# Optimization experiments

Measured on AMD Instinct MI355X. Metric: run time of the kernel, lower is better.

Reference implementation:

```python
import jax, jax.numpy as jnp
import numpy as np

N_NODES = 100000
HIDDEN = 128


def gcn_conv(x, edge_index, W, b, n_nodes):
    """PyG GCNConv: out = D^{-1/2} (A+I) D^{-1/2} (x @ W) + b."""
    src, dst = edge_index[0], edge_index[1]
    # add self-loops
    loop = jnp.arange(n_nodes, dtype=src.dtype)
    src = jnp.concatenate([src, loop])
    dst = jnp.concatenate([dst, loop])
    # degree of (A + I) w.r.t. destination nodes
    deg = jax.ops.segment_sum(jnp.ones_like(dst, dtype=x.dtype), dst,
                              num_segments=n_nodes)
    dinv = jax.lax.rsqrt(jnp.where(deg > 0, deg, 1.0))
    norm = dinv[src] * dinv[dst]  # [E+N]
    h = x @ W                      # [N, F_out]
    msg = h[src] * norm[:, None]   # gather + scale, [E+N, F_out]
    out = jax.ops.segment_sum(msg, dst, num_segments=n_nodes)
    return out + b


def setup_inputs() -> dict:
    key = jax.random.key(0)
    k1, k2, k3, k4, k5, k6 = jax.random.split(key, 6)
    num_features, num_classes = 128, 40
    n_edges = 1600000
    x = jax.random.normal(k1, (N_NODES, num_features), dtype=jnp.float32)
    edge_index = jax.random.randint(k2, (2, n_edges), 0, N_NODES, dtype=jnp.int64)
    s1 = 1.0 / np.sqrt(num_features)
    s2 = 1.0 / np.sqrt(HIDDEN)
    W1 = jax.random.uniform(k3, (num_features, HIDDEN), jnp.float32, -s1, s1)
    b1 = jax.random.uniform(k4, (HIDDEN,), jnp.float32, -s1, s1)
    W2 = jax.random.uniform(k5, (HIDDEN, num_classes), jnp.float32, -s2, s2)
    b2 = jax.random.uniform(k6, (num_classes,), jnp.float32, -s2, s2)
    return {"x": x, "edge_index": edge_index, "W1": W1, "b1": b1,
            "W2": W2, "b2": b2}


def reference(x, edge_index, W1, b1, W2, b2):
    n = x.shape[0]
    h = gcn_conv(x, edge_index, W1, b1, n)
    h = jax.nn.relu(h)
    # dropout is identity in eval mode (training=False)
    out = gcn_conv(h, edge_index, W2, b2, n)
    return out
```

## Files before the change

kernel.cpp:

```cpp
#include <hip/hip_runtime.h>


__device__ inline unsigned pack_bf16(float a, float b) {
  unsigned ua = __float_as_uint(a), ub = __float_as_uint(b);
  ua += 0x7fffu + ((ua >> 16) & 1u);
  ub += 0x7fffu + ((ub >> 16) & 1u);
  return (ua >> 16) | (ub & 0xffff0000u);
}
__device__ inline float unpack_lo(unsigned u) { return __uint_as_float(u << 16); }
__device__ inline float unpack_hi(unsigned u) { return __uint_as_float(u & 0xffff0000u); }


__global__ void kb_count(const int* __restrict__ dst, int E,
                         int* __restrict__ bucket_cnt, int NB) {
  __shared__ int h[256];
  h[threadIdx.x] = 0;
  __syncthreads();
  int i = blockIdx.x * blockDim.x + threadIdx.x;
  int stride = gridDim.x * blockDim.x;
  for (; i < E; i += stride) atomicAdd(&h[dst[i] >> 9], 1);
  __syncthreads();
  if (threadIdx.x < NB && h[threadIdx.x]) atomicAdd(&bucket_cnt[threadIdx.x], h[threadIdx.x]);
}

__global__ void kb_scan(const int* __restrict__ bucket_cnt, int NB, int E,
                        int* __restrict__ bucket_start, int* __restrict__ bucket_cursor) {
  int tid = threadIdx.x, lane = tid & 63, w = tid >> 6;
  int v = (tid < NB) ? bucket_cnt[tid] : 0;
  int x = v;
#pragma unroll
  for (int off = 1; off < 64; off <<= 1) {
    int u = __shfl_up(x, off);
    if (lane >= off) x += u;
  }
  __shared__ int ws4[4];
  if (lane == 63) ws4[w] = x;
  __syncthreads();
  int add = 0;
  for (int k = 0; k < w; ++k) add += ws4[k];
  x += add;
  int excl = x - v;
  if (tid < NB) {
    bucket_start[tid] = excl;
    bucket_cursor[tid] = excl;
  }
  if (tid == 0) bucket_start[NB] = E;
}

__global__ __launch_bounds__(256) void kb_scatter(const int* __restrict__ src,
                                                  const int* __restrict__ dst, int E,
                                                  int* __restrict__ bucket_cursor,
                                                  unsigned* __restrict__ pairs) {
  constexpr int T = 16;
  __shared__ int bin_cnt[256], bin_base[256];
  bin_cnt[threadIdx.x] = 0;
  __syncthreads();
  int base = blockIdx.x * (256 * T);
  unsigned u[T];
  int bb[T], slot[T];
#pragma unroll
  for (int t = 0; t < T; ++t) {
    int e = base + t * 256 + threadIdx.x;
    if (e < E) {
      int s = src[e], d = dst[e];
      bb[t] = d >> 9;
      u[t] = (unsigned)s | ((unsigned)(d & 511) << 17);
      slot[t] = atomicAdd(&bin_cnt[bb[t]], 1);
    } else {
      bb[t] = -1;
    }
  }
  __syncthreads();
  if (bin_cnt[threadIdx.x] > 0)
    bin_base[threadIdx.x] = atomicAdd(&bucket_cursor[threadIdx.x], bin_cnt[threadIdx.x]);
  __syncthreads();
#pragma unroll
  for (int t = 0; t < T; ++t)
    if (bb[t] >= 0) pairs[bin_base[bb[t]] + slot[t]] = u[t];
}

__global__ __launch_bounds__(256) void kc_csr(const unsigned* __restrict__ pairs,
                                              const int* __restrict__ bucket_start,
                                              int N, float* __restrict__ dinv,
                                              int* __restrict__ row_start,
                                              int* __restrict__ deg,
                                              int* __restrict__ col) {
  int b = blockIdx.x;
  int pbase = bucket_start[b], m = bucket_start[b + 1] - pbase;
  int tid = threadIdx.x, lane = tid & 63, w = tid >> 6;
  __shared__ int cnt[512], cur[512];
  __shared__ int ws4[4];
  cnt[tid] = 0;
  cnt[tid + 256] = 0;
  __syncthreads();
  for (int i = tid; i < m; i += 256) atomicAdd(&cnt[pairs[pbase + i] >> 17], 1);
  __syncthreads();
  int c0 = cnt[2 * tid], c1 = cnt[2 * tid + 1];
  int p = c0 + c1, x = p;
#pragma unroll
  for (int off = 1; off < 64; off <<= 1) {
    int uu = __shfl_up(x, off);
    if (lane >= off) x += uu;
  }
  if (lane == 63) ws4[w] = x;
  __syncthreads();
  int add = 0;
  for (int k = 0; k < w; ++k) add += ws4[k];
  x += add;
  int xe = x - p;
  cur[2 * tid] = xe;
  cur[2 * tid + 1] = xe + c0;
  int n0 = b * 512 + 2 * tid;
  if (n0 < N) {
    deg[n0] = c0;
    dinv[n0] = rsqrtf((float)(c0 + 1));
    row_start[n0] = pbase + xe;
  }
  if (n0 + 1 < N) {
    deg[n0 + 1] = c1;
    dinv[n0 + 1] = rsqrtf((float)(c1 + 1));
    row_start[n0 + 1] = pbase + xe + c0;
  }
  __syncthreads();
  for (int i = tid; i < m; i += 256) {
    unsigned uu = pairs[pbase + i];
    int pos = atomicAdd(&cur[uu >> 17], 1);
    col[pbase + pos] = (int)(uu & 131071u);
  }
}


template <int CT, int RPT, int NC, int KP>
__global__ __launch_bounds__(256, 4) void k_gemm_t(const float* __restrict__ X,
                                                   const float* __restrict__ W,
                                                   const float* __restrict__ dinv,
                                                   unsigned* __restrict__ G,
                                                   int N) {
  constexpr int K = 128;
  constexpr int LDX = K + 4;
  constexpr int RT = 256 / CT;
  constexpr int RB = RT * RPT;
  constexpr int PHASES = K / KP;
  constexpr int KV = K / 4;

  __shared__ float Wl[KP * NC];
  __shared__ float Xl[RB * LDX];

  const int tid = threadIdx.x;
  const int row0 = blockIdx.x * RB;

  const float4* X4 = (const float4*)(X + (size_t)row0 * K);
  if (row0 + RB <= N) {
#pragma unroll
    for (int i = tid; i < RB * KV; i += 256) {
      int r = i / KV, c = i % KV;
      *(float4*)&Xl[r * LDX + c * 4] = X4[i];
    }
  } else {
    int lim = (N - row0) * KV;
    for (int i = tid; i < RB * KV; i += 256) {
      int r = i / KV, c = i % KV;
      *(float4*)&Xl[r * LDX + c * 4] =
          (i < lim) ? X4[i] : float4{0.f, 0.f, 0.f, 0.f};
    }
  }

  const int cx = tid % CT;
  const int ry = tid / CT;
  const int c0 = cx * 4;
  const bool cact = (c0 < NC);
  const int c0c = cact ? c0 : 0;

  float acc[RPT][4];
#pragma unroll
  for (int j = 0; j < RPT; ++j)
#pragma unroll
    for (int c = 0; c < 4; ++c) acc[j][c] = 0.f;

  for (int p = 0; p < PHASES; ++p) {
    constexpr int WV = KP * NC / 4;
    const float4* W4 = (const float4*)(W + (size_t)p * KP * NC);
    float4* Wl4 = (float4*)Wl;
    if (p > 0) __syncthreads();
#pragma unroll
    for (int i = tid; i < WV; i += 256) Wl4[i] = W4[i];
    __syncthreads();

#pragma unroll 2
    for (int k4 = 0; k4 < KP / 4; ++k4) {
      float4 xv[RPT], wv[4];
#pragma unroll
      for (int j = 0; j < RPT; ++j)
        xv[j] = *(const float4*)&Xl[(ry * RPT + j) * LDX + p * KP + k4 * 4];
#pragma unroll
      for (int kk = 0; kk < 4; ++kk)
        wv[kk] = *(const float4*)&Wl[(k4 * 4 + kk) * NC + c0c];
#pragma unroll
      for (int kk = 0; kk < 4; ++kk)
#pragma unroll
        for (int j = 0; j < RPT; ++j) {
          float xs = ((const float*)&xv[j])[kk];
#pragma unroll
          for (int c = 0; c < 4; ++c)
            acc[j][c] = fmaf(xs, ((const float*)&wv[kk])[c], acc[j][c]);
        }
    }
  }

  if (cact) {
#pragma unroll
    for (int j = 0; j < RPT; ++j) {
      int r = row0 + ry * RPT + j;
      if (r < N) {
        float d = dinv[r];
        uint2 o;
        o.x = pack_bf16(acc[j][0] * d, acc[j][1] * d);
        o.y = pack_bf16(acc[j][2] * d, acc[j][3] * d);
        *(uint2*)&G[(size_t)r * (NC / 2) + c0 / 2] = o;
      }
    }
  }
}


__global__ void k_agg1(const unsigned* __restrict__ g1, const int* __restrict__ row_start,
                       const int* __restrict__ deg, const int* __restrict__ col,
                       const float* __restrict__ dinv, const float* __restrict__ b1,
                       float* __restrict__ h2, int N) {
  int node = blockIdx.x * 4 + (threadIdx.x >> 6);
  if (node >= N) return;
  int lane = threadIdx.x & 63;
  unsigned su = g1[(size_t)node * 64 + lane];
  float ax = unpack_lo(su), ay = unpack_hi(su);
  int start = row_start[node], cnt = deg[node];
  int j = 0;
  for (; j + 8 <= cnt; j += 8) {
    unsigned u[8];
#pragma unroll
    for (int t = 0; t < 8; ++t)
      u[t] = g1[(size_t)col[start + j + t] * 64 + lane];
#pragma unroll
    for (int t = 0; t < 8; ++t) {
      ax += unpack_lo(u[t]);
      ay += unpack_hi(u[t]);
    }
  }
  for (; j + 4 <= cnt; j += 4) {
    unsigned u[4];
#pragma unroll
    for (int t = 0; t < 4; ++t)
      u[t] = g1[(size_t)col[start + j + t] * 64 + lane];
#pragma unroll
    for (int t = 0; t < 4; ++t) {
      ax += unpack_lo(u[t]);
      ay += unpack_hi(u[t]);
    }
  }
  for (; j < cnt; ++j) {
    unsigned u = g1[(size_t)col[start + j] * 64 + lane];
    ax += unpack_lo(u);
    ay += unpack_hi(u);
  }
  float dn = dinv[node];
  float2 bb = ((const float2*)b1)[lane];
  float2 o;
  o.x = fmaxf(fmaf(ax, dn, bb.x), 0.f);
  o.y = fmaxf(fmaf(ay, dn, bb.y), 0.f);
  ((float2*)h2)[(size_t)node * 64 + lane] = o;
}


__global__ void k_agg2(const unsigned* __restrict__ g2, const int* __restrict__ row_start,
                       const int* __restrict__ deg, const int* __restrict__ col,
                       const float* __restrict__ dinv, const float* __restrict__ b2,
                       float* __restrict__ out, int N) {
  int node = blockIdx.x * 4 + (threadIdx.x >> 6);
  if (node >= N) return;
  int lane = threadIdx.x & 63;
  if (lane >= 20) return;
  unsigned su = g2[(size_t)node * 20 + lane];
  float ax = unpack_lo(su), ay = unpack_hi(su);
  int start = row_start[node], cnt = deg[node];
  int j = 0;
  for (; j + 8 <= cnt; j += 8) {
    unsigned u[8];
#pragma unroll
    for (int t = 0; t < 8; ++t)
      u[t] = g2[(size_t)col[start + j + t] * 20 + lane];
#pragma unroll
    for (int t = 0; t < 8; ++t) {
      ax += unpack_lo(u[t]);
      ay += unpack_hi(u[t]);
    }
  }
  for (; j < cnt; ++j) {
    unsigned u = g2[(size_t)col[start + j] * 20 + lane];
    ax += unpack_lo(u);
    ay += unpack_hi(u);
  }
  float dn = dinv[node];
  float2 o;
  o.x = fmaf(ax, dn, b2[2 * lane]);
  o.y = fmaf(ay, dn, b2[2 * lane + 1]);
  *(float2*)&out[(size_t)node * 40 + 2 * lane] = o;
}


extern "C" void kernel_launch(void* const* d_in, const int* in_sizes, int n_in,
                              void* d_out, int out_size, void* d_ws, size_t ws_size,
                              hipStream_t stream) {
  const float* x = (const float*)d_in[0];
  const int* ei = (const int*)d_in[1];
  const float* W1 = (const float*)d_in[2];
  const float* b1 = (const float*)d_in[3];
  const float* W2 = (const float*)d_in[4];
  const float* b2 = (const float*)d_in[5];

  const int F = in_sizes[3];
  const int N = in_sizes[0] / F;
  const int E = in_sizes[1] / 2;
  const int* esrc = ei;
  const int* edst = ei + E;
  const int NB = (N + 511) / 512;

  char* ws = (char*)d_ws;
  int* bucket_cnt = (int*)(ws + 0);
  int* bucket_start = (int*)(ws + 4096);
  int* bucket_cursor = (int*)(ws + 8192);
  float* dinv = (float*)(ws + 16384);
  int* row_start = (int*)(ws + 417792);
  int* deg = (int*)(ws + 819200);
  unsigned* pairs = (unsigned*)(ws + 1220608);
  int* colx = (int*)(ws + 7621632);
  unsigned* g1 = (unsigned*)(ws + 14680064);
  float* h2 = (float*)(ws + 41943040);
  unsigned* g2 = g1;

  hipMemsetAsync(bucket_cnt, 0, 1024, stream);

  kb_count<<<256, 256, 0, stream>>>(edst, E, bucket_cnt, NB);
  kb_scan<<<1, 256, 0, stream>>>(bucket_cnt, NB, E, bucket_start, bucket_cursor);
  kb_scatter<<<(E + 4095) / 4096, 256, 0, stream>>>(esrc, edst, E, bucket_cursor, pairs);
  kc_csr<<<NB, 256, 0, stream>>>(pairs, bucket_start, N, dinv, row_start, deg, colx);

  k_gemm_t<32, 4, 128, 64><<<3125, 256, 0, stream>>>(x, W1, dinv, g1, N);
  k_agg1<<<(N + 3) / 4, 256, 0, stream>>>(g1, row_start, deg, colx, dinv, b1, h2, N);
  k_gemm_t<16, 2, 40, 128><<<3125, 256, 0, stream>>>(h2, W2, dinv, g2, N);
  k_agg2<<<(N + 3) / 4, 256, 0, stream>>>(g2, row_start, deg, colx, dinv, b2,
                                          (float*)d_out, N);
}
```

Measured before the change: 366.8 us.

## Use bf16 MFMA for both GCN GEMMs and store hidden layer as bf16

Replaces the scalar-FMA fp32 tiled GEMMs with a kernel that uses 16x16x32 bf16 MFMA instructions. Weights are pre-transposed and packed to bf16 by a small kernel, and X is converted to bf16 while loading into LDS. The first aggregation now writes the hidden activations as packed bf16, which halves the h2 write and the second GEMM's read. This trades fp32 accuracy in the GEMM inputs for matrix-core throughput and less memory traffic.

```diff
diff --git a/kernel.cpp b/kernel.cpp
--- a/kernel.cpp
+++ b/kernel.cpp
@@ -1,4 +1,7 @@
 #include <hip/hip_runtime.h>
+
+typedef short s16x8 __attribute__((ext_vector_type(8)));
+typedef float f32x4 __attribute__((ext_vector_type(4)));
 
 
 __device__ inline unsigned pack_bf16(float a, float b) {
@@ -130,94 +133,94 @@
 }
 
 
-template <int CT, int RPT, int NC, int KP>
-__global__ __launch_bounds__(256, 4) void k_gemm_t(const float* __restrict__ X,
-                                                   const float* __restrict__ W,
-                                                   const float* __restrict__ dinv,
-                                                   unsigned* __restrict__ G,
-                                                   int N) {
-  constexpr int K = 128;
-  constexpr int LDX = K + 4;
-  constexpr int RT = 256 / CT;
-  constexpr int RB = RT * RPT;
-  constexpr int PHASES = K / KP;
-  constexpr int KV = K / 4;
-
-  __shared__ float Wl[KP * NC];
-  __shared__ float Xl[RB * LDX];
+__global__ void kw_trans(const float* __restrict__ W, int NC, int NT,
+                         unsigned* __restrict__ WT) {
+  int id = blockIdx.x * 256 + threadIdx.x;
+  if (id >= NT * 64) return;
+  int n = id >> 6, kd = id & 63;
+  float a = 0.f, b = 0.f;
+  if (n < NC) {
+    a = W[(2 * kd) * NC + n];
+    b = W[(2 * kd + 1) * NC + n];
+  }
+  WT[id] = pack_bf16(a, b);
+}
+
+
+template <int NTILES, int GSTRIDE, int NCOLS, bool A_FP32>
+__global__ __launch_bounds__(256, 4) void k_gemm_mfma(const void* __restrict__ Ain,
+                                                      const unsigned* __restrict__ WT,
+                                                      const float* __restrict__ dinv,
+                                                      unsigned* __restrict__ G, int N) {
+  __shared__ unsigned Ws[NTILES * 16 * 68];
+  __shared__ unsigned As[64 * 68];
 
   const int tid = threadIdx.x;
-  const int row0 = blockIdx.x * RB;
-
-  const float4* X4 = (const float4*)(X + (size_t)row0 * K);
-  if (row0 + RB <= N) {
-#pragma unroll
-    for (int i = tid; i < RB * KV; i += 256) {
-      int r = i / KV, c = i % KV;
-      *(float4*)&Xl[r * LDX + c * 4] = X4[i];
+  const int row0 = blockIdx.x * 64;
+
+  constexpr int WV2 = NTILES * 16 * 32;
+  const uint2* WT2 = (const uint2*)WT;
+#pragma unroll
+  for (int i = tid; i < WV2; i += 256) {
+    int r = i >> 5, kd2 = i & 31;
+    *(uint2*)&Ws[r * 68 + kd2 * 2] = WT2[i];
+  }
+
+  if (A_FP32) {
+    const float4* X4 = (const float4*)Ain + (size_t)row0 * 32;
+#pragma unroll
+    for (int i = tid; i < 2048; i += 256) {
+      int r = i >> 5, c4 = i & 31;
+      uint2 o = {0u, 0u};
+      if (row0 + r < N) {
+        float4 xv = X4[i];
+        o.x = pack_bf16(xv.x, xv.y);
+        o.y = pack_bf16(xv.z, xv.w);
+      }
+      *(uint2*)&As[r * 68 + c4 * 2] = o;
     }
   } else {
-    int lim = (N - row0) * KV;
-    for (int i = tid; i < RB * KV; i += 256) {
-      int r = i / KV, c = i % KV;
-      *(float4*)&Xl[r * LDX + c * 4] =
-          (i < lim) ? X4[i] : float4{0.f, 0.f, 0.f, 0.f};
-    }
-  }
-
-  const int cx = tid % CT;
-  const int ry = tid / CT;
-  const int c0 = cx * 4;
-  const bool cact = (c0 < NC);
-  const int c0c = cact ? c0 : 0;
-
-  float acc[RPT][4];
-#pragma unroll
-  for (int j = 0; j < RPT; ++j)
-#pragma unroll
-    for (int c = 0; c < 4; ++c) acc[j][c] = 0.f;
-
-  for (int p = 0; p < PHASES; ++p) {
-    constexpr int WV = KP * NC / 4;
-    const float4* W4 = (const float4*)(W + (size_t)p * KP * NC);
-    float4* Wl4 = (float4*)Wl;
-    if (p > 0) __syncthreads();
-#pragma unroll
-    for (int i = tid; i < WV; i += 256) Wl4[i] = W4[i];
-    __syncthreads();
-
-#pragma unroll 2
-    for (int k4 = 0; k4 < KP / 4; ++k4) {
-      float4 xv[RPT], wv[4];
-#pragma unroll
-      for (int j = 0; j < RPT; ++j)
-        xv[j] = *(const float4*)&Xl[(ry * RPT + j) * LDX + p * KP + k4 * 4];
-#pragma unroll
-      for (int kk = 0; kk < 4; ++kk)
-        wv[kk] = *(const float4*)&Wl[(k4 * 4 + kk) * NC + c0c];
-#pragma unroll
-      for (int kk = 0; kk < 4; ++kk)
-#pragma unroll
-        for (int j = 0; j < RPT; ++j) {
-          float xs = ((const float*)&xv[j])[kk];
-#pragma unroll
-          for (int c = 0; c < 4; ++c)
-            acc[j][c] = fmaf(xs, ((const float*)&wv[kk])[c], acc[j][c]);
-        }
-    }
-  }
-
-  if (cact) {
-#pragma unroll
-    for (int j = 0; j < RPT; ++j) {
-      int r = row0 + ry * RPT + j;
-      if (r < N) {
-        float d = dinv[r];
-        uint2 o;
-        o.x = pack_bf16(acc[j][0] * d, acc[j][1] * d);
-        o.y = pack_bf16(acc[j][2] * d, acc[j][3] * d);
-        *(uint2*)&G[(size_t)r * (NC / 2) + c0 / 2] = o;
-      }
+    const uint2* H2 = (const uint2*)Ain + (size_t)row0 * 32;
+#pragma unroll
+    for (int i = tid; i < 2048; i += 256) {
+      int r = i >> 5, kd2 = i & 31;
+      uint2 o = {0u, 0u};
+      if (row0 + r < N) o = H2[i];
+      *(uint2*)&As[r * 68 + kd2 * 2] = o;
+    }
+  }
+  __syncthreads();
+
+  const int w = tid >> 6, lane = tid & 63;
+  const int quad = lane >> 4, n16 = lane & 15;
+
+  f32x4 acc[NTILES];
+#pragma unroll
+  for (int t = 0; t < NTILES; ++t) acc[t] = {0.f, 0.f, 0.f, 0.f};
+
+  const char* Ab = (const char*)As + (w * 16 + n16) * 272 + quad * 16;
+  const char* Bb = (const char*)Ws + n16 * 272 + quad * 16;
+#pragma unroll
+  for (int s = 0; s < 4; ++s) {
+    s16x8 a = *(const s16x8*)(Ab + s * 64);
+#pragma unroll
+    for (int t = 0; t < NTILES; ++t) {
+      s16x8 b = *(const s16x8*)(Bb + t * 16 * 272 + s * 64);
+      acc[t] = __builtin_amdgcn_mfma_f32_16x16x32_bf16(a, b, acc[t], 0, 0, 0);
+    }
+  }
+
+#pragma unroll
+  for (int reg = 0; reg < 4; ++reg) {
+    int r = row0 + w * 16 + quad * 4 + reg;
+    float dv = (r < N) ? dinv[r] : 0.f;
+#pragma unroll
+    for (int t = 0; t < NTILES; ++t) {
+      float v = acc[t][reg] * dv;
+      float vp = __shfl_xor(v, 1);
+      int colc = t * 16 + n16;
+      if ((n16 & 1) == 0 && colc < NCOLS && r < N)
+        G[(size_t)r * GSTRIDE + t * 8 + (n16 >> 1)] = pack_bf16(v, vp);
     }
   }
 }
@@ -226,7 +229,7 @@
 __global__ void k_agg1(const unsigned* __restrict__ g1, const int* __restrict__ row_start,
                        const int* __restrict__ deg, const int* __restrict__ col,
                        const float* __restrict__ dinv, const float* __restrict__ b1,
-                       float* __restrict__ h2, int N) {
+                       unsigned* __restrict__ h2, int N) {
   int node = blockIdx.x * 4 + (threadIdx.x >> 6);
   if (node >= N) return;
   int lane = threadIdx.x & 63;
@@ -263,10 +266,9 @@
   }
   float dn = dinv[node];
   float2 bb = ((const float2*)b1)[lane];
-  float2 o;
-  o.x = fmaxf(fmaf(ax, dn, bb.x), 0.f);
-  o.y = fmaxf(fmaf(ay, dn, bb.y), 0.f);
-  ((float2*)h2)[(size_t)node * 64 + lane] = o;
+  float ox = fmaxf(fmaf(ax, dn, bb.x), 0.f);
+  float oy = fmaxf(fmaf(ay, dn, bb.y), 0.f);
+  h2[(size_t)node * 64 + lane] = pack_bf16(ox, oy);
 }
 
 
@@ -327,13 +329,15 @@
   int* bucket_cnt = (int*)(ws + 0);
   int* bucket_start = (int*)(ws + 4096);
   int* bucket_cursor = (int*)(ws + 8192);
-  float* dinv = (float*)(ws + 16384);
-  int* row_start = (int*)(ws + 417792);
-  int* deg = (int*)(ws + 819200);
-  unsigned* pairs = (unsigned*)(ws + 1220608);
-  int* colx = (int*)(ws + 7621632);
-  unsigned* g1 = (unsigned*)(ws + 14680064);
-  float* h2 = (float*)(ws + 41943040);
+  unsigned* w1t = (unsigned*)(ws + 16384);
+  unsigned* w2t = (unsigned*)(ws + 49152);
+  float* dinv = (float*)(ws + 65536);
+  int* row_start = (int*)(ws + 466944);
+  int* deg = (int*)(ws + 868352);
+  unsigned* pairs = (unsigned*)(ws + 1269760);
+  int* colx = (int*)(ws + 7669760);
+  unsigned* g1 = (unsigned*)(ws + 14073856);
+  unsigned* h2 = (unsigned*)(ws + 39673856);
   unsigned* g2 = g1;
 
   hipMemsetAsync(bucket_cnt, 0, 1024, stream);
@@ -343,9 +347,13 @@
   kb_scatter<<<(E + 4095) / 4096, 256, 0, stream>>>(esrc, edst, E, bucket_cursor, pairs);
   kc_csr<<<NB, 256, 0, stream>>>(pairs, bucket_start, N, dinv, row_start, deg, colx);
 
-  k_gemm_t<32, 4, 128, 64><<<3125, 256, 0, stream>>>(x, W1, dinv, g1, N);
+  kw_trans<<<32, 256, 0, stream>>>(W1, 128, 128, w1t);
+  kw_trans<<<12, 256, 0, stream>>>(W2, 40, 48, w2t);
+
+  const int gblocks = (N + 63) / 64;
+  k_gemm_mfma<8, 64, 128, true><<<gblocks, 256, 0, stream>>>(x, w1t, dinv, g1, N);
   k_agg1<<<(N + 3) / 4, 256, 0, stream>>>(g1, row_start, deg, colx, dinv, b1, h2, N);
-  k_gemm_t<16, 2, 40, 128><<<3125, 256, 0, stream>>>(h2, W2, dinv, g2, N);
+  k_gemm_mfma<3, 20, 40, false><<<gblocks, 256, 0, stream>>>(h2, w2t, dinv, g2, N);
   k_agg2<<<(N + 3) / 4, 256, 0, stream>>>(g2, row_start, deg, colx, dinv, b2,
                                           (float*)d_out, N);
 }
```

New measurement: 326.5 us. 1.12x faster.
